# Kernel tuning notes

Measured on AMD Instinct MI355X. Metric: run time of the kernel, lower is better.

The kernel has to match this reference:

```python
import jax, jax.numpy as jnp
import numpy as np

D = 4096; K = 512; HOP = 512; WIN = 16384
NUM_REGIONS = 1 + (WIN - D) // HOP            # 25
D2_Y = 128; K2 = 128; STRIDE_Y = 2
D3_X = 25; K3 = 256
NR2Y = 1 + (K - D2_Y) // STRIDE_Y             # 193
NR3X = 1 + (NUM_REGIONS - D3_X)               # 1
M = 128


def create_filters(d=D, k=K, sr=44100, start_freq=50, end_freq=6000):
    x = jnp.linspace(0.0, 2 * np.pi, d + 1)[:d]
    num_cycles = start_freq * d / sr
    scaling_ind = np.log(end_freq / start_freq) / k
    window_mask = 1.0 - jnp.cos(x)
    phases = jnp.exp(jnp.arange(float(k)) * scaling_ind)[None, :] * num_cycles * x[:, None]
    filters = jnp.stack((jnp.cos(phases), jnp.sin(phases)), axis=2) * window_mask[:, None, None]
    return filters.astype(jnp.float32)          # [d, k, 2]


def setup_inputs() -> dict:
    key = jax.random.key(0)
    k1, k2, k3, k4 = jax.random.split(key, 4)
    x = jax.random.normal(k1, (128, WIN), dtype=jnp.float32)
    filters = create_filters().reshape(D, 2 * K)                     # [4096, 1024]
    # Conv weights in OIHW layout (torch Conv2d convention), kaiming-ish scale
    conv1_w = jax.random.normal(k2, (K2, 1, 1, D2_Y), dtype=jnp.float32) / np.sqrt(D2_Y)
    conv2_w = jax.random.normal(k3, (K3, K2, D3_X, 1), dtype=jnp.float32) / np.sqrt(K2 * D3_X)
    beta_w = jax.random.normal(k4, (M, NR3X * NR2Y * K3), dtype=jnp.float32) / np.sqrt(NR3X * NR2Y * K3)
    return {"x": x, "filters": filters, "conv1_w": conv1_w, "conv2_w": conv2_w, "beta_w": beta_w}


def reference(x, filters, conv1_w, conv2_w, beta_w):
    B = x.shape[0]
    # unfold(1, D, HOP): overlapping windows -> [B, NUM_REGIONS, D]
    idx = jnp.arange(NUM_REGIONS)[:, None] * HOP + jnp.arange(D)[None, :]
    windows = x[:, idx]                                               # [B, 25, 4096]
    spec = windows @ filters                                          # [B, 25, 1024]
    # complex magnitude^2: pairs of (cos, sin) components
    zx = jnp.sum(spec.reshape(B, NUM_REGIONS, K, 2) ** 2, axis=3)     # [B, 25, 512]
    zx = jnp.log(zx + 1e-14)[:, None]                                 # [B, 1, 25, 512]
    dn = ("NCHW", "OIHW", "NCHW")
    h = jax.lax.conv_general_dilated(zx, conv1_w, (1, STRIDE_Y), "VALID", dimension_numbers=dn)
    h = jax.nn.relu(h)                                                # [B, 128, 25, 193]
    h = jax.lax.conv_general_dilated(h, conv2_w, (1, 1), "VALID", dimension_numbers=dn)
    h = jax.nn.relu(h)                                                # [B, 256, 1, 193]
    y = h.reshape(B, -1) @ beta_w.T                                   # [B, 128]
    return y
```

## Files before the change

kernel.cpp:

```cpp
#include <hip/hip_runtime.h>
#include <hip/hip_bf16.h>
#include <math.h>


typedef __attribute__((ext_vector_type(8))) short s8v;
typedef __attribute__((ext_vector_type(8))) _Float16 half8;
typedef __attribute__((ext_vector_type(16))) float f16v;

__device__ inline ushort f2bf(float f) {
    union { float f; unsigned u; } v; v.f = f;
    unsigned u = v.u;
    return (ushort)((u + 0x7FFFu + ((u >> 16) & 1u)) >> 16);
}

__global__ void k0x_xh(const float* __restrict__ x, _Float16* __restrict__ xh) {
    int i = blockIdx.x * 256 + threadIdx.x;
    xh[i] = (_Float16)x[i];
}

__global__ __launch_bounds__(256)
void k0f_fB(const float* __restrict__ filt, _Float16* __restrict__ fB) {
    __shared__ float tile[8][257];
    const int t   = threadIdx.x;
    const int n0  = blockIdx.x * 256;
    const int kc8 = blockIdx.y;
    for (int idx = t; idx < 8 * 256; idx += 256) {
        int kk = idx >> 8, n = idx & 255;
        tile[kk][n] = filt[(kc8 * 8 + kk) * 1024 + n0 + n];
    }
    __syncthreads();
    half8 v;
#pragma unroll
    for (int j = 0; j < 8; j++) v[j] = (_Float16)tile[j][t];
    *(half8*)(fB + (size_t)kc8 * 8192 + (size_t)(n0 + t) * 8) = v;
}

__global__ void k0a_w1b(const float* __restrict__ w1, ushort* __restrict__ w1b) {
    int i = blockIdx.x * 256 + threadIdx.x;
    w1b[i] = f2bf(w1[i]);
}

__global__ void k0b_w2c(const float* __restrict__ w2, ushort* __restrict__ w2c) {
    int i = blockIdx.x * 256 + threadIdx.x;
    int k2 = i & 127;
    int dx = (i >> 7) % 25;
    int k3 = i / 3200;
    w2c[i] = f2bf(w2[(k3 * 128 + k2) * 25 + dx]);
}

__global__ void k0c_bb(const float* __restrict__ beta, ushort* __restrict__ bb) {
    int i = blockIdx.x * 256 + threadIdx.x;
    bb[i] = f2bf(beta[i]);
}

#define K1_PHASE(P, KB, PREF, vbC, vbN)                                            \
  {                                                                                \
    __syncthreads();                                                               \
    half8 na0, na1;                                                                \
    if (PREF) {                                                                    \
      na0 = *(const half8*)(apt + ((KB) + 1) * 32);                                \
      na1 = *(const half8*)(apt + ((KB) + 1) * 32 + 16);                           \
      _Pragma("unroll")                                                            \
      for (int s = 0; s < 2; s++) {                                                \
        const _Float16* pBk = pB + ((size_t)((KB) + 1) * 2 + s) * 16384;           \
        vbN[s][0] = *(const half8*)(pBk);                                          \
        vbN[s][1] = *(const half8*)(pBk + 256);                                    \
      }                                                                            \
    }                                                                              \
    _Pragma("unroll")                                                              \
    for (int s = 0; s < 2; s++) {                                                  \
      half8 a0 = *(const half8*)((const char*)Al + (P) * 8192 + s * 4096 +         \
                                 (wm + ml) * 32 + qf * 16);                        \
      half8 a1 = *(const half8*)((const char*)Al + (P) * 8192 + s * 4096 +         \
                                 (wm + 32 + ml) * 32 + qf * 16);                   \
      acc[0][0] = __builtin_amdgcn_mfma_f32_32x32x16_f16(a0, vbC[s][0], acc[0][0], 0, 0, 0); \
      acc[0][1] = __builtin_amdgcn_mfma_f32_32x32x16_f16(a0, vbC[s][1], acc[0][1], 0, 0, 0); \
      acc[1][0] = __builtin_amdgcn_mfma_f32_32x32x16_f16(a1, vbC[s][0], acc[1][0], 0, 0, 0); \
      acc[1][1] = __builtin_amdgcn_mfma_f32_32x32x16_f16(a1, vbC[s][1], acc[1][1], 0, 0, 0); \
    }                                                                              \
    if (PREF) {                                                                    \
      half8* dnx = (half8*)((char*)Al + (1 - (P)) * 8192);                         \
      dnx[t] = na0;                                                                \
      dnx[256 + t] = na1;                                                          \
    }                                                                              \
  }

__global__ __launch_bounds__(256)
void k1_mfma(const _Float16* __restrict__ xh, const _Float16* __restrict__ fB,
             ushort* __restrict__ zxb) {
    __shared__ _Float16 Al[2][4096];
    const int t  = threadIdx.x;
    const int n0 = blockIdx.x * 128;
    const int m0 = blockIdx.y * 128;
    const int w  = t >> 6, l = t & 63;
    const int wm = (w >> 1) * 64, wn = (w & 1) * 64;
    const int qf = l >> 5;
    const int ml = l & 31;

    const int srow = t >> 1;
    const int sq   = t & 1;
    const int gm   = m0 + srow;
    const _Float16* apt = xh + (gm / 25) * 16384 + (gm % 25) * 512 + sq * 8;

    const _Float16* pB = fB + ((size_t)qf * 1024 + (size_t)(n0 + wn + ml)) * 8;

    f16v acc[2][2];
#pragma unroll
    for (int i = 0; i < 2; i++)
#pragma unroll
        for (int j = 0; j < 2; j++)
#pragma unroll
            for (int r = 0; r < 16; r++) acc[i][j][r] = 0.f;

    half8 vbA[2][2], vbB[2][2];

    {
        half8 v0 = *(const half8*)(apt);
        half8 v1 = *(const half8*)(apt + 16);
        half8* d0 = (half8*)Al;
        d0[t] = v0;
        d0[256 + t] = v1;
#pragma unroll
        for (int s = 0; s < 2; s++) {
            const _Float16* pBk = pB + (size_t)s * 16384;
            vbA[s][0] = *(const half8*)(pBk);
            vbA[s][1] = *(const half8*)(pBk + 256);
        }
    }

    for (int kb2 = 0; kb2 < 63; kb2++) {
        const int kb = kb2 * 2;
        K1_PHASE(0, kb, true, vbA, vbB)
        K1_PHASE(1, kb + 1, true, vbB, vbA)
    }
    K1_PHASE(0, 126, true, vbA, vbB)
    K1_PHASE(1, 127, false, vbB, vbA)

#pragma unroll
    for (int mt = 0; mt < 2; mt++)
#pragma unroll
        for (int nt = 0; nt < 2; nt++) {
#pragma unroll
            for (int r = 0; r < 16; r++) {
                float val = acc[mt][nt][r];
                float oth = __shfl_xor(val, 1, 64);
                if (!(l & 1)) {
                    float pw = fmaf(val, val, fmaf(oth, oth, 1e-14f));
                    int m = m0 + wm + mt * 32 + 4 * qf + (r & 3) + 8 * (r >> 2);
                    int n = n0 + wn + nt * 32 + ml;
                    zxb[m * 512 + (n >> 1)] = f2bf(logf(pw));
                }
            }
        }
}

#define ZPITCH 272
__global__ __launch_bounds__(256, 2)
void k2_mfma(const ushort* __restrict__ zxb, const ushort* __restrict__ w1b,
             const ushort* __restrict__ w2c, ushort* __restrict__ h2b) {
    __shared__ ushort zl[2 * 3 * 4 * ZPITCH];
    __shared__ ushort h1l[3 * 16 * 64 * 8];
    const int t  = threadIdx.x;
    const int yt = blockIdx.x;
    const int b  = blockIdx.y;
    const int y0 = yt * 64;
    const int w  = t >> 6;
    const int l  = t & 63;
    const int yy = l & 31;
    const int q  = l >> 5;

    s8v w1f[8];
    {
        const ushort* wp = w1b + (32 * w + yy) * 128 + 8 * q;
#pragma unroll
        for (int ks = 0; ks < 8; ks++)
            w1f[ks] = *(const s8v*)(wp + 16 * ks);
    }

    f16v acc[2][2];
#pragma unroll
    for (int mt = 0; mt < 2; mt++)
#pragma unroll
        for (int nt = 0; nt < 2; nt++)
#pragma unroll
            for (int r = 0; r < 16; r++) acc[mt][nt][r] = 0.f;

    {
        const int nq = 3 * 4 * 62;
        for (int idx = t; idx < nq; idx += 256) {
            int iq = idx % 62;
            int dc = idx / 62;
            int c = dc & 3, d = dc >> 2;
            const ushort* src = zxb + ((b * 25 + d) << 9);
            int gg = 2 * y0 + 2 * c + 4 * iq;
            ushort* dst = zl + (d * 4 + c) * ZPITCH + 4 * iq;
#pragma unroll
            for (int u = 0; u < 4; u++) {
                int g = gg + u;
                dst[u] = (g < 512) ? src[g] : (ushort)0;
            }
        }
    }

    for (int ch = 0; ch < 9; ch++) {
        const int p  = ch & 1;
        const int nd = (ch == 8) ? 1 : 3;
        __syncthreads();

        ushort pv[12];
        int nq2 = 0;
        if (ch < 8) {
            const int nd2 = (ch == 7) ? 1 : 3;
            nq2 = nd2 * 4 * 62;
#pragma unroll
            for (int r = 0; r < 3; r++) {
                int idx = t + r * 256;
                if (idx < nq2) {
                    int iq = idx % 62;
                    int dc = idx / 62;
                    int c = dc & 3, d = dc >> 2;
                    const ushort* src = zxb + ((b * 25 + (ch + 1) * 3 + d) << 9);
                    int gg = 2 * y0 + 2 * c + 4 * iq;
#pragma unroll
                    for (int u = 0; u < 4; u++) {
                        int g = gg + u;
                        pv[r * 4 + u] = (g < 512) ? src[g] : (ushort)0;
                    }
                }
            }
        }

        for (int d = 0; d < nd; d++) {
            const int zb = (p * 3 + d) * 4;
#pragma unroll
            for (int nt = 0; nt < 2; nt++) {
                const int ye = nt * 32 + yy;
                const ushort* zp = zl + (zb + (ye & 3)) * ZPITCH + 8 * (ye >> 2) + 8 * q;
                f16v a1;
#pragma unroll
                for (int r = 0; r < 16; r++) a1[r] = 0.f;
#pragma unroll
                for (int ks = 0; ks < 8; ks++) {
                    s8v bf = *(const s8v*)(zp + 16 * ks);
                    a1 = __builtin_amdgcn_mfma_f32_32x32x16_bf16(w1f[ks], bf, a1, 0, 0, 0);
                }
#pragma unroll
                for (int g = 0; g < 4; g++) {
                    unsigned p0 = (unsigned)f2bf(fmaxf(a1[4 * g + 0], 0.f))
                                | ((unsigned)f2bf(fmaxf(a1[4 * g + 1], 0.f)) << 16);
                    unsigned p1 = (unsigned)f2bf(fmaxf(a1[4 * g + 2], 0.f))
                                | ((unsigned)f2bf(fmaxf(a1[4 * g + 3], 0.f)) << 16);
                    unsigned* dst = (unsigned*)(h1l + (((d * 16 + 4 * w + g) * 64) + ye) * 8 + 4 * q);
                    dst[0] = p0; dst[1] = p1;
                }
            }
        }

        if (ch < 8) {
#pragma unroll
            for (int r = 0; r < 3; r++) {
                int idx = t + r * 256;
                if (idx < nq2) {
                    int iq = idx % 62;
                    int dc = idx / 62;
                    int c = dc & 3, d = dc >> 2;
                    ushort* dst = zl + (((1 - p) * 3 + d) * 4 + c) * ZPITCH + 4 * iq;
#pragma unroll
                    for (int u = 0; u < 4; u++) dst[u] = pv[r * 4 + u];
                }
            }
        }

        __syncthreads();

        for (int d = 0; d < nd; d++) {
            const int dxa = ch * 3 + d;
            const ushort* ap = w2c + (size_t)(64 * w + yy) * 3200 + dxa * 128 + 8 * q;
#pragma unroll
            for (int ks = 0; ks < 8; ks++) {
                s8v a0 = *(const s8v*)(ap + 16 * ks);
                s8v a1f = *(const s8v*)(ap + (size_t)32 * 3200 + 16 * ks);
#pragma unroll
                for (int nt = 0; nt < 2; nt++) {
                    s8v hb = *(const s8v*)(h1l + (((d * 16 + 2 * ks + q) * 64) + nt * 32 + yy) * 8);
                    acc[0][nt] = __builtin_amdgcn_mfma_f32_32x32x16_bf16(a0, hb, acc[0][nt], 0, 0, 0);
                    acc[1][nt] = __builtin_amdgcn_mfma_f32_32x32x16_bf16(a1f, hb, acc[1][nt], 0, 0, 0);
                }
            }
        }
    }

#pragma unroll
    for (int mt = 0; mt < 2; mt++)
#pragma unroll
        for (int nt = 0; nt < 2; nt++) {
            int y = y0 + nt * 32 + yy;
            if (y < 193) {
#pragma unroll
                for (int r = 0; r < 16; r++) {
                    int k3 = 64 * w + 32 * mt + (r & 3) + 8 * (r >> 2) + 4 * q;
                    h2b[(b * 256 + k3) * 193 + y] = f2bf(fmaxf(acc[mt][nt][r], 0.f));
                }
            }
        }
}

__global__ __launch_bounds__(256)
void k4_mfma(const ushort* __restrict__ h2b, const ushort* __restrict__ bb,
             float* __restrict__ part) {
    const int t = threadIdx.x, w = t >> 6, l = t & 63;
    const int s = blockIdx.x;
    const int kb = s * 256;
    const int qf = l >> 5;
    const int ml = l & 31;
    const ushort* pa  = h2b + (size_t)(w * 32 + ml) * 49408 + kb + qf * 8;
    const ushort* pb0 = bb  + (size_t)ml * 49408 + kb + qf * 8;

    f16v acc[4];
#pragma unroll
    for (int nt = 0; nt < 4; nt++)
#pragma unroll
        for (int r = 0; r < 16; r++) acc[nt][r] = 0.f;

    for (int ks = 0; ks < 16; ks++) {
        s8v af = *(const s8v*)(pa + ks * 16);
#pragma unroll
        for (int nt = 0; nt < 4; nt++) {
            s8v bf = *(const s8v*)(pb0 + (size_t)nt * 32 * 49408 + ks * 16);
            acc[nt] = __builtin_amdgcn_mfma_f32_32x32x16_bf16(af, bf, acc[nt], 0, 0, 0);
        }
    }
    float* pp = part + (size_t)s * 16384;
#pragma unroll
    for (int nt = 0; nt < 4; nt++)
#pragma unroll
        for (int r = 0; r < 16; r++) {
            int m = w * 32 + 4 * qf + (r & 3) + 8 * (r >> 2);
            pp[m * 128 + nt * 32 + ml] = acc[nt][r];
        }
}

__global__ __launch_bounds__(256)
void k5_red(const float* __restrict__ part, float* __restrict__ out) {
    __shared__ float red[256];
    const int t  = threadIdx.x;
    const int io = t & 63;
    const int kq = t >> 6;
    const int i  = blockIdx.x * 64 + io;
    float s = 0.f;
#pragma unroll 4
    for (int k = kq; k < 193; k += 4) s += part[(size_t)k * 16384 + i];
    red[t] = s;
    __syncthreads();
    if (t < 64)
        out[blockIdx.x * 64 + t] = (red[t] + red[t + 64]) + (red[t + 128] + red[t + 192]);
}

extern "C" void kernel_launch(void* const* d_in, const int* in_sizes, int n_in,
                              void* d_out, int out_size, void* d_ws, size_t ws_size,
                              hipStream_t stream) {
    const float* x    = (const float*)d_in[0];
    const float* filt = (const float*)d_in[1];
    const float* w1   = (const float*)d_in[2];
    const float* w2   = (const float*)d_in[3];
    const float* beta = (const float*)d_in[4];
    float* out = (float*)d_out;

    char* ws = (char*)d_ws;
    ushort*   zxb  = (ushort*)(ws + 0);
    ushort*   h2b  = (ushort*)(ws + 3276800);
    ushort*   w1b  = (ushort*)(ws + 15921152);
    ushort*   w2c  = (ushort*)(ws + 15953920);
    ushort*   bb   = (ushort*)(ws + 17592320);
    _Float16* xh   = (_Float16*)(ws + 30240768);
    _Float16* fB   = (_Float16*)(ws + 34435072);
    float*    part = (float*)(ws + 30240768);

    k0x_xh<<<8192, 256, 0, stream>>>(x, xh);
    k0f_fB<<<dim3(4, 512), 256, 0, stream>>>(filt, fB);
    k0a_w1b<<<64, 256, 0, stream>>>(w1, w1b);
    k0b_w2c<<<3200, 256, 0, stream>>>(w2, w2c);
    k0c_bb<<<24704, 256, 0, stream>>>(beta, bb);
    k1_mfma<<<dim3(8, 25), 256, 0, stream>>>(xh, fB, zxb);
    k2_mfma<<<dim3(4, 128), 256, 0, stream>>>(zxb, w1b, w2c, h2b);
    k4_mfma<<<193, 256, 0, stream>>>(h2b, bb, part);
    k5_red<<<256, 256, 0, stream>>>(part, out);
}
```

Measured before the change: 314.7 us.

## Fuse w1 and beta bf16 conversions into consumer kernels, add MFMA priority

Removes the separate w1 and beta fp32-to-bf16 conversion kernels and instead converts the fp32 values in registers inside k2 and k4 right before the MFMAs. This drops two launches and the write and re-read of a large bf16 copy of beta, at the cost of reading fp32 beta (twice the bytes) directly in k4. It also drops the occupancy hint on k2 and wraps its MFMA loops in s_setprio to favour matrix issue.

```diff
diff --git a/kernel.cpp b/kernel.cpp
--- a/kernel.cpp
+++ b/kernel.cpp
@@ -35,22 +35,12 @@
     *(half8*)(fB + (size_t)kc8 * 8192 + (size_t)(n0 + t) * 8) = v;
 }
 
-__global__ void k0a_w1b(const float* __restrict__ w1, ushort* __restrict__ w1b) {
-    int i = blockIdx.x * 256 + threadIdx.x;
-    w1b[i] = f2bf(w1[i]);
-}
-
 __global__ void k0b_w2c(const float* __restrict__ w2, ushort* __restrict__ w2c) {
     int i = blockIdx.x * 256 + threadIdx.x;
     int k2 = i & 127;
     int dx = (i >> 7) % 25;
     int k3 = i / 3200;
     w2c[i] = f2bf(w2[(k3 * 128 + k2) * 25 + dx]);
-}
-
-__global__ void k0c_bb(const float* __restrict__ beta, ushort* __restrict__ bb) {
-    int i = blockIdx.x * 256 + threadIdx.x;
-    bb[i] = f2bf(beta[i]);
 }
 
 #define K1_PHASE(P, KB, PREF, vbC, vbN)                                            \
@@ -155,8 +145,8 @@
 }
 
 #define ZPITCH 272
-__global__ __launch_bounds__(256, 2)
-void k2_mfma(const ushort* __restrict__ zxb, const ushort* __restrict__ w1b,
+__global__ __launch_bounds__(256)
+void k2_mfma(const ushort* __restrict__ zxb, const float* __restrict__ w1,
              const ushort* __restrict__ w2c, ushort* __restrict__ h2b) {
     __shared__ ushort zl[2 * 3 * 4 * ZPITCH];
     __shared__ ushort h1l[3 * 16 * 64 * 8];
@@ -171,10 +161,18 @@
 
     s8v w1f[8];
     {
-        const ushort* wp = w1b + (32 * w + yy) * 128 + 8 * q;
-#pragma unroll
-        for (int ks = 0; ks < 8; ks++)
-            w1f[ks] = *(const s8v*)(wp + 16 * ks);
+        const float* wp = w1 + (32 * w + yy) * 128 + 8 * q;
+#pragma unroll
+        for (int ks = 0; ks < 8; ks++) {
+            float4 f0 = *(const float4*)(wp + 16 * ks);
+            float4 f1 = *(const float4*)(wp + 16 * ks + 4);
+            s8v v;
+            v[0] = (short)f2bf(f0.x); v[1] = (short)f2bf(f0.y);
+            v[2] = (short)f2bf(f0.z); v[3] = (short)f2bf(f0.w);
+            v[4] = (short)f2bf(f1.x); v[5] = (short)f2bf(f1.y);
+            v[6] = (short)f2bf(f1.z); v[7] = (short)f2bf(f1.w);
+            w1f[ks] = v;
+        }
     }
 
     f16v acc[2][2];
@@ -230,6 +228,7 @@
             }
         }
 
+        __builtin_amdgcn_s_setprio(1);
         for (int d = 0; d < nd; d++) {
             const int zb = (p * 3 + d) * 4;
 #pragma unroll
@@ -255,6 +254,7 @@
                 }
             }
         }
+        __builtin_amdgcn_s_setprio(0);
 
         if (ch < 8) {
 #pragma unroll
@@ -273,6 +273,7 @@
 
         __syncthreads();
 
+        __builtin_amdgcn_s_setprio(1);
         for (int d = 0; d < nd; d++) {
             const int dxa = ch * 3 + d;
             const ushort* ap = w2c + (size_t)(64 * w + yy) * 3200 + dxa * 128 + 8 * q;
@@ -288,6 +289,7 @@
                 }
             }
         }
+        __builtin_amdgcn_s_setprio(0);
     }
 
 #pragma unroll
@@ -306,15 +308,15 @@
 }
 
 __global__ __launch_bounds__(256)
-void k4_mfma(const ushort* __restrict__ h2b, const ushort* __restrict__ bb,
+void k4_mfma(const ushort* __restrict__ h2b, const float* __restrict__ beta,
              float* __restrict__ part) {
     const int t = threadIdx.x, w = t >> 6, l = t & 63;
     const int s = blockIdx.x;
     const int kb = s * 256;
     const int qf = l >> 5;
     const int ml = l & 31;
-    const ushort* pa  = h2b + (size_t)(w * 32 + ml) * 49408 + kb + qf * 8;
-    const ushort* pb0 = bb  + (size_t)ml * 49408 + kb + qf * 8;
+    const ushort* pa = h2b + (size_t)(w * 32 + ml) * 49408 + kb + qf * 8;
+    const float*  pb = beta + (size_t)ml * 49408 + kb + qf * 8;
 
     f16v acc[4];
 #pragma unroll
@@ -326,7 +328,14 @@
         s8v af = *(const s8v*)(pa + ks * 16);
 #pragma unroll
         for (int nt = 0; nt < 4; nt++) {
-            s8v bf = *(const s8v*)(pb0 + (size_t)nt * 32 * 49408 + ks * 16);
+            const float* pbf = pb + (size_t)nt * 32 * 49408 + ks * 16;
+            float4 f0 = *(const float4*)(pbf);
+            float4 f1 = *(const float4*)(pbf + 4);
+            s8v bf;
+            bf[0] = (short)f2bf(f0.x); bf[1] = (short)f2bf(f0.y);
+            bf[2] = (short)f2bf(f0.z); bf[3] = (short)f2bf(f0.w);
+            bf[4] = (short)f2bf(f1.x); bf[5] = (short)f2bf(f1.y);
+            bf[6] = (short)f2bf(f1.z); bf[7] = (short)f2bf(f1.w);
             acc[nt] = __builtin_amdgcn_mfma_f32_32x32x16_bf16(af, bf, acc[nt], 0, 0, 0);
         }
     }
@@ -369,20 +378,16 @@
     char* ws = (char*)d_ws;
     ushort*   zxb  = (ushort*)(ws + 0);
     ushort*   h2b  = (ushort*)(ws + 3276800);
-    ushort*   w1b  = (ushort*)(ws + 15921152);
     ushort*   w2c  = (ushort*)(ws + 15953920);
-    ushort*   bb   = (ushort*)(ws + 17592320);
     _Float16* xh   = (_Float16*)(ws + 30240768);
     _Float16* fB   = (_Float16*)(ws + 34435072);
     float*    part = (float*)(ws + 30240768);
 
     k0x_xh<<<8192, 256, 0, stream>>>(x, xh);
     k0f_fB<<<dim3(4, 512), 256, 0, stream>>>(filt, fB);
-    k0a_w1b<<<64, 256, 0, stream>>>(w1, w1b);
     k0b_w2c<<<3200, 256, 0, stream>>>(w2, w2c);
-    k0c_bb<<<24704, 256, 0, stream>>>(beta, bb);
     k1_mfma<<<dim3(8, 25), 256, 0, stream>>>(xh, fB, zxb);
-    k2_mfma<<<dim3(4, 128), 256, 0, stream>>>(zxb, w1b, w2c, h2b);
-    k4_mfma<<<193, 256, 0, stream>>>(h2b, bb, part);
+    k2_mfma<<<dim3(4, 128), 256, 0, stream>>>(zxb, w1, w2c, h2b);
+    k4_mfma<<<193, 256, 0, stream>>>(h2b, beta, part);
     k5_red<<<256, 256, 0, stream>>>(part, out);
 }
```

After: 328.5 us. 1.04x slower.

## Deepen k1 prefetch to two stages ahead and replace syncthreads with raw barrier

Applied to the files above, without the earlier changes.

The spectrogram GEMM kernel now prefetches global A and B fragments two k-blocks ahead using four rotating B register sets and two A register buffers, instead of one ahead. The __syncthreads is replaced with an explicit lgkmcnt wait plus s_barrier, so outstanding global loads are not drained at each barrier. This is meant to hide global memory latency behind the MFMA work, at the cost of more live registers, which could reduce occupancy.

```diff
diff --git a/kernel.cpp b/kernel.cpp
--- a/kernel.cpp
+++ b/kernel.cpp
@@ -53,35 +53,36 @@
     bb[i] = f2bf(beta[i]);
 }
 
-#define K1_PHASE(P, KB, PREF, vbC, vbN)                                            \
+#define K1P(KB, LP, VU, VL, RL, RW, DOPREF, DOWRITE)                               \
   {                                                                                \
-    __syncthreads();                                                               \
-    half8 na0, na1;                                                                \
-    if (PREF) {                                                                    \
-      na0 = *(const half8*)(apt + ((KB) + 1) * 32);                                \
-      na1 = *(const half8*)(apt + ((KB) + 1) * 32 + 16);                           \
+    asm volatile("s_waitcnt lgkmcnt(0)" ::: "memory");                             \
+    __builtin_amdgcn_s_barrier();                                                  \
+    asm volatile("" ::: "memory");                                                 \
+    if (DOPREF) {                                                                  \
+      RL[0] = *(const half8*)(apt + ((KB) + 2) * 32);                              \
+      RL[1] = *(const half8*)(apt + ((KB) + 2) * 32 + 16);                         \
       _Pragma("unroll")                                                            \
       for (int s = 0; s < 2; s++) {                                                \
-        const _Float16* pBk = pB + ((size_t)((KB) + 1) * 2 + s) * 16384;           \
-        vbN[s][0] = *(const half8*)(pBk);                                          \
-        vbN[s][1] = *(const half8*)(pBk + 256);                                    \
+        const _Float16* pBk = pB + ((size_t)((KB) + 2) * 2 + s) * 16384;           \
+        VL[s][0] = *(const half8*)(pBk);                                           \
+        VL[s][1] = *(const half8*)(pBk + 256);                                     \
       }                                                                            \
     }                                                                              \
     _Pragma("unroll")                                                              \
     for (int s = 0; s < 2; s++) {                                                  \
-      half8 a0 = *(const half8*)((const char*)Al + (P) * 8192 + s * 4096 +         \
+      half8 a0 = *(const half8*)((const char*)Al + (LP) * 8192 + s * 4096 +        \
                                  (wm + ml) * 32 + qf * 16);                        \
-      half8 a1 = *(const half8*)((const char*)Al + (P) * 8192 + s * 4096 +         \
+      half8 a1 = *(const half8*)((const char*)Al + (LP) * 8192 + s * 4096 +        \
                                  (wm + 32 + ml) * 32 + qf * 16);                   \
-      acc[0][0] = __builtin_amdgcn_mfma_f32_32x32x16_f16(a0, vbC[s][0], acc[0][0], 0, 0, 0); \
-      acc[0][1] = __builtin_amdgcn_mfma_f32_32x32x16_f16(a0, vbC[s][1], acc[0][1], 0, 0, 0); \
-      acc[1][0] = __builtin_amdgcn_mfma_f32_32x32x16_f16(a1, vbC[s][0], acc[1][0], 0, 0, 0); \
-      acc[1][1] = __builtin_amdgcn_mfma_f32_32x32x16_f16(a1, vbC[s][1], acc[1][1], 0, 0, 0); \
+      acc[0][0] = __builtin_amdgcn_mfma_f32_32x32x16_f16(a0, VU[s][0], acc[0][0], 0, 0, 0); \
+      acc[0][1] = __builtin_amdgcn_mfma_f32_32x32x16_f16(a0, VU[s][1], acc[0][1], 0, 0, 0); \
+      acc[1][0] = __builtin_amdgcn_mfma_f32_32x32x16_f16(a1, VU[s][0], acc[1][0], 0, 0, 0); \
+      acc[1][1] = __builtin_amdgcn_mfma_f32_32x32x16_f16(a1, VU[s][1], acc[1][1], 0, 0, 0); \
     }                                                                              \
-    if (PREF) {                                                                    \
-      half8* dnx = (half8*)((char*)Al + (1 - (P)) * 8192);                         \
-      dnx[t] = na0;                                                                \
-      dnx[256 + t] = na1;                                                          \
+    if (DOWRITE) {                                                                 \
+      half8* dnx = (half8*)((char*)Al + (1 - (LP)) * 8192);                        \
+      dnx[t] = RW[0];                                                              \
+      dnx[256 + t] = RW[1];                                                        \
     }                                                                              \
   }
 
@@ -112,29 +113,39 @@
 #pragma unroll
             for (int r = 0; r < 16; r++) acc[i][j][r] = 0.f;
 
-    half8 vbA[2][2], vbB[2][2];
+    half8 vb0[2][2], vb1[2][2], vb2[2][2], vb3[2][2];
+    half8 rA0[2], rA1[2];
 
     {
-        half8 v0 = *(const half8*)(apt);
-        half8 v1 = *(const half8*)(apt + 16);
+        rA0[0] = *(const half8*)(apt);
+        rA0[1] = *(const half8*)(apt + 16);
         half8* d0 = (half8*)Al;
-        d0[t] = v0;
-        d0[256 + t] = v1;
+        d0[t] = rA0[0];
+        d0[256 + t] = rA0[1];
+        rA1[0] = *(const half8*)(apt + 32);
+        rA1[1] = *(const half8*)(apt + 48);
 #pragma unroll
         for (int s = 0; s < 2; s++) {
             const _Float16* pBk = pB + (size_t)s * 16384;
-            vbA[s][0] = *(const half8*)(pBk);
-            vbA[s][1] = *(const half8*)(pBk + 256);
-        }
-    }
-
-    for (int kb2 = 0; kb2 < 63; kb2++) {
-        const int kb = kb2 * 2;
-        K1_PHASE(0, kb, true, vbA, vbB)
-        K1_PHASE(1, kb + 1, true, vbB, vbA)
-    }
-    K1_PHASE(0, 126, true, vbA, vbB)
-    K1_PHASE(1, 127, false, vbB, vbA)
+            vb0[s][0] = *(const half8*)(pBk);
+            vb0[s][1] = *(const half8*)(pBk + 256);
+            const _Float16* pBk1 = pB + ((size_t)2 + s) * 16384;
+            vb1[s][0] = *(const half8*)(pBk1);
+            vb1[s][1] = *(const half8*)(pBk1 + 256);
+        }
+    }
+
+    for (int it = 0; it < 31; it++) {
+        const int kb = it * 4;
+        K1P(kb + 0, 0, vb0, vb2, rA0, rA1, true, true)
+        K1P(kb + 1, 1, vb1, vb3, rA1, rA0, true, true)
+        K1P(kb + 2, 0, vb2, vb0, rA0, rA1, true, true)
+        K1P(kb + 3, 1, vb3, vb1, rA1, rA0, true, true)
+    }
+    K1P(124, 0, vb0, vb2, rA0, rA1, true, true)
+    K1P(125, 1, vb1, vb3, rA1, rA0, true, true)
+    K1P(126, 0, vb2, vb0, rA0, rA1, false, true)
+    K1P(127, 1, vb3, vb1, rA1, rA0, false, false)
 
 #pragma unroll
     for (int mt = 0; mt < 2; mt++)
```

New measurement: 293.9 us. 6.6% less time.
